# Kernel tuning notes

Hardware: AMD Instinct MI355X
Metric: run time of the kernel (lower is better)

The kernel has to match this reference:

```python
import jax, jax.numpy as jnp
import numpy as np


def setup_inputs() -> dict:
    key = jax.random.key(0)
    ks = jax.random.split(key, 6)
    B, S, D, E = 8, 4096, 4096, 64
    lim = 1.0 / np.sqrt(D)  # nn.Linear default init range
    return {
        "h": jax.random.normal(ks[0], (B, S, D), dtype=jnp.float32),
        "Ww": jax.random.uniform(ks[1], (E, D), dtype=jnp.float32, minval=-lim, maxval=lim),
        "bw": jax.random.uniform(ks[2], (E,), dtype=jnp.float32, minval=-lim, maxval=lim),
        "Wn": jax.random.uniform(ks[3], (E, D), dtype=jnp.float32, minval=-lim, maxval=lim),
        "bn": jax.random.uniform(ks[4], (E,), dtype=jnp.float32, minval=-lim, maxval=lim),
        "noise": jax.random.normal(ks[5], (B, S, E), dtype=jnp.float32),
        "top_k": 8,
    }


def reference(h, Ww, bw, Wn, bn, noise, top_k):
    B, S, E = h.shape[0], h.shape[1], Ww.shape[0]
    logits = jnp.einsum("bsd,ed->bse", h, Ww) + bw           # lin_w(h)
    noise_scale = jax.nn.softplus(jnp.einsum("bsd,ed->bse", h, Wn) + bn)  # softplus(lin_n(h))
    noisy = logits + noise * noise_scale
    full = jax.nn.softmax(noisy, axis=-1)
    topk, ix = jax.lax.top_k(noisy, top_k)                    # [B,S,k]
    # scatter topk values into a -inf tensor along the expert axis
    flat_noisy = noisy.reshape(-1, E)
    rows = jnp.arange(flat_noisy.shape[0])[:, None]           # [BS,1]
    sparse = jnp.full_like(flat_noisy, -jnp.inf).at[rows, ix.reshape(-1, top_k)].set(
        topk.reshape(-1, top_k))
    gates = jax.nn.softmax(sparse, axis=-1).reshape(B, S, E)
    return gates, ix, full
```

## Files before the change

kernel.cpp:

```cpp
#include <hip/hip_runtime.h>
#include <hip/hip_bf16.h>
#include <math.h>


typedef __attribute__((ext_vector_type(8))) _Float16 f16x8;
typedef __attribute__((ext_vector_type(4))) float f32x4;
typedef unsigned int u32;

#define BM 64
#define D_DIM 4096
#define NSTEP 128
#define WSTEP_BYTES 16384

#define BUF_BYTES 24576
#define SMEM_BYTES 49152

__device__ __forceinline__ float softplus_f(float x) {
    return fmaxf(x, 0.0f) + log1pf(expf(-fabsf(x)));
}

__device__ __forceinline__ void gl16(void* lds, const void* g) {
    __builtin_amdgcn_global_load_lds(
        (const __attribute__((address_space(1))) u32*)g,
        (__attribute__((address_space(3))) u32*)lds, 16, 0, 0);
}

#define MFMA16F(A, B, C) __builtin_amdgcn_mfma_f32_16x16x32_f16((A), (B), (C), 0, 0, 0)

__global__ __launch_bounds__(256)
void wconv_kernel(const float* __restrict__ Ww, const float* __restrict__ Wn,
                  char* __restrict__ Wp)
{
    const int bid = blockIdx.x;
    const int kc = bid >> 1, half = bid & 1;
    const int t = threadIdx.x;
    const int vrow = half * 64 + (t >> 2);
    const int c4 = t & 3;
    const float* src = (vrow < 64) ? (Ww + (size_t)vrow * D_DIM)
                                   : (Wn + (size_t)(vrow - 64) * D_DIM);
    const float4 a = *reinterpret_cast<const float4*>(src + kc * 32 + c4 * 8);
    const float4 b = *reinterpret_cast<const float4*>(src + kc * 32 + c4 * 8 + 4);
    const float f[8] = {a.x, a.y, a.z, a.w, b.x, b.y, b.z, b.w};
    union { _Float16 h[8]; uint4 q; } P0, P1;
#pragma unroll
    for (int i = 0; i < 8; ++i) {
        _Float16 lo = (_Float16)f[i];
        P0.h[i] = lo;
        P1.h[i] = (_Float16)((f[i] - (float)lo) * 2048.0f);
    }
    const int sc = c4 ^ ((vrow >> 2) & 3);
    char* dst = Wp + (size_t)kc * WSTEP_BYTES + vrow * 64 + sc * 16;
    *reinterpret_cast<uint4*>(dst)        = P0.q;
    *reinterpret_cast<uint4*>(dst + 8192) = P1.q;
}

__global__ __launch_bounds__(512, 4)
void router_kernel(const float* __restrict__ h,
                   const float* __restrict__ bw,
                   const float* __restrict__ bn,
                   const float* __restrict__ noise,
                   const char* __restrict__ Wp,
                   float* __restrict__ out_gates,
                   float* __restrict__ out_ix,
                   float* __restrict__ out_full)
{
    __shared__ __align__(16) char smem[SMEM_BYTES];

    const int t    = threadIdx.x;
    const int row0 = blockIdx.x * BM;
    const int lane = t & 63, w = t >> 6;
    const int c = lane & 15, kg = lane >> 4;
    const int wr = w >> 2, wc = w & 3;

    const int hl  = lane >> 3;
    const int hsc = (lane & 7) ^ hl;
    const float* hsrc = h + (size_t)(row0 + w * 8 + hl) * D_DIM + hsc * 4;
    const int hdst = w * 1024;
    const char* wsrc = Wp + w * 1024 + lane * 16;

    f32x4 grp[2][2], sA[2][2], accM[2][2], accM2[2][2];
#pragma unroll
    for (int fi = 0; fi < 2; ++fi)
#pragma unroll
        for (int j = 0; j < 2; ++j) {
            grp[fi][j] = (f32x4)0.0f; sA[fi][j] = (f32x4)0.0f;
            accM[fi][j] = (f32x4)0.0f; accM2[fi][j] = (f32x4)0.0f;
        }

    gl16(smem + hdst, hsrc);
    gl16(smem + 8192 + w * 1024, wsrc);
    gl16(smem + 8192 + 8192 + w * 1024, wsrc + 8192);
    __syncthreads();

    int cur = 0;
    for (int kc = 0; kc < NSTEP; ++kc) {
        if (kc + 1 < NSTEP) {
            char* nb = smem + (cur ^ 1) * BUF_BYTES;
            gl16(nb + hdst, hsrc + (size_t)(kc + 1) * 32);
            const char* ws = wsrc + (size_t)(kc + 1) * WSTEP_BYTES;
            gl16(nb + 8192 + w * 1024, ws);
            gl16(nb + 16384 + w * 1024, ws + 8192);
        }

        const char* hb = smem + cur * BUF_BYTES;
        const char* wb = hb + 8192;

        f16x8 A0[2], A1[2];
#pragma unroll
        for (int fi = 0; fi < 2; ++fi) {
            const int arow = wr * 32 + fi * 16 + c;
            const int s0 = ((kg * 2)     ^ (arow & 7)) * 16;
            const int s1 = ((kg * 2 + 1) ^ (arow & 7)) * 16;
            const float4 fa = *reinterpret_cast<const float4*>(hb + arow * 128 + s0);
            const float4 fb = *reinterpret_cast<const float4*>(hb + arow * 128 + s1);
            const float f[8] = {fa.x, fa.y, fa.z, fa.w, fb.x, fb.y, fb.z, fb.w};
#pragma unroll
            for (int i = 0; i < 8; ++i) {
                _Float16 lo = (_Float16)f[i];
                A0[fi][i] = lo;
                A1[fi][i] = (_Float16)((f[i] - (float)lo) * 2048.0f);
            }
        }

#pragma unroll
        for (int j = 0; j < 2; ++j) {
            const int brow = wc * 32 + j * 16 + c;
            const int bo = brow * 64 + ((kg ^ ((brow >> 2) & 3)) * 16);
            const f16x8 B0 = *reinterpret_cast<const f16x8*>(wb + bo);
            const f16x8 B1 = *reinterpret_cast<const f16x8*>(wb + bo + 8192);
#pragma unroll
            for (int fi = 0; fi < 2; ++fi) {
                grp[fi][j]   = MFMA16F(A0[fi], B0, grp[fi][j]);
                accM[fi][j]  = MFMA16F(A0[fi], B1, accM[fi][j]);
                accM[fi][j]  = MFMA16F(A1[fi], B0, accM[fi][j]);
                accM2[fi][j] = MFMA16F(A1[fi], B1, accM2[fi][j]);
            }
        }

        if ((kc & 15) == 15) {
#pragma unroll
            for (int fi = 0; fi < 2; ++fi)
#pragma unroll
                for (int j = 0; j < 2; ++j) {
#pragma unroll
                    for (int e = 0; e < 4; ++e) sA[fi][j][e] += grp[fi][j][e];
                    grp[fi][j] = (f32x4)0.0f;
                }
        }

        __syncthreads();
        cur ^= 1;
    }

    float* lw_s = reinterpret_cast<float*>(smem);
    float* ln_s = lw_s + 64 * 65;
    float* dst = (wc < 2) ? lw_s : ln_s;
#pragma unroll
    for (int fi = 0; fi < 2; ++fi)
#pragma unroll
        for (int j = 0; j < 2; ++j)
#pragma unroll
            for (int r = 0; r < 4; ++r) {
                const int rowl = wr * 32 + fi * 16 + kg * 4 + r;
                const int e = (wc & 1) * 32 + j * 16 + c;
                dst[rowl * 65 + e] = sA[fi][j][r]
                                   + accM[fi][j][r]  * 4.8828125e-4f
                                   + accM2[fi][j][r] * 2.384185791015625e-7f;
            }
    __syncthreads();

    const float bwv = bw[lane];
    const float bnv = bn[lane];
    for (int q = 0; q < 8; ++q) {
        const int lrow = w * 8 + q;
        const int grow = row0 + lrow;
        const float lwv = lw_s[lrow * 65 + lane] + bwv;
        const float lnv = ln_s[lrow * 65 + lane] + bnv;
        const float nz  = noise[(size_t)grow * 64 + lane];
        const float v   = lwv + nz * softplus_f(lnv);

        float cur2 = v;
        float m8 = 0.0f;
        int winIdx = 0;
        bool picked = false;
#pragma unroll
        for (int r = 0; r < 8; ++r) {
            float bvv = cur2;
            int   bi  = lane;
#pragma unroll
            for (int off = 32; off; off >>= 1) {
                const float ov = __shfl_xor(bvv, off);
                const int   oi = __shfl_xor(bi, off);
                if (ov > bvv || (ov == bvv && oi < bi)) { bvv = ov; bi = oi; }
            }
            if (r == 0) m8 = bvv;
            if (lane == r) winIdx = bi;
            if (lane == bi) { picked = true; cur2 = -INFINITY; }
        }

        const float pf = expf(v - m8);
        const float pg = picked ? pf : 0.0f;
        float sf = pf, sg = pg;
#pragma unroll
        for (int off = 32; off; off >>= 1) {
            sf += __shfl_xor(sf, off);
            sg += __shfl_xor(sg, off);
        }

        out_full [(size_t)grow * 64 + lane] = pf / sf;
        out_gates[(size_t)grow * 64 + lane] = pg / sg;
        if (lane < 8) out_ix[(size_t)grow * 8 + lane] = (float)winIdx;
    }
}

extern "C" void kernel_launch(void* const* d_in, const int* in_sizes, int n_in,
                              void* d_out, int out_size, void* d_ws, size_t ws_size,
                              hipStream_t stream) {
    const float* h  = (const float*)d_in[0];
    const float* Ww = (const float*)d_in[1];
    const float* bw = (const float*)d_in[2];
    const float* Wn = (const float*)d_in[3];
    const float* bn = (const float*)d_in[4];
    const float* nz = (const float*)d_in[5];

    const int rows = in_sizes[5] / 64;

    float* out = (float*)d_out;
    float* og = out;
    float* oi = out + (size_t)rows * 64;
    float* of = out + (size_t)rows * 64 + (size_t)rows * 8;

    char* Wp = (char*)d_ws;

    hipLaunchKernelGGL(wconv_kernel, dim3(256), dim3(256), 0, stream, Ww, Wn, Wp);
    hipLaunchKernelGGL(router_kernel, dim3(rows / BM), dim3(512), 0, stream,
                       h, bw, bn, nz, Wp, og, oi, of);
}
```

Before: 249.7 us.

## Triple-buffer LDS loads with partial waitcnt and drop lo*lo MFMA term

Measured after the change: 242.7 us, median of 2. 1.03x faster.

```diff
diff --git a/kernel.cpp b/kernel.cpp
--- a/kernel.cpp
+++ b/kernel.cpp
@@ -13,7 +13,7 @@
 #define WSTEP_BYTES 16384
 
 #define BUF_BYTES 24576
-#define SMEM_BYTES 49152
+#define SMEM_BYTES 73728
 
 __device__ __forceinline__ float softplus_f(float x) {
     return fmaxf(x, 0.0f) + log1pf(expf(-fabsf(x)));
@@ -78,31 +78,38 @@
     const int hdst = w * 1024;
     const char* wsrc = Wp + w * 1024 + lane * 16;
 
-    f32x4 grp[2][2], sA[2][2], accM[2][2], accM2[2][2];
+    f32x4 grp[2][2], sA[2][2], accM[2][2];
 #pragma unroll
     for (int fi = 0; fi < 2; ++fi)
 #pragma unroll
         for (int j = 0; j < 2; ++j) {
             grp[fi][j] = (f32x4)0.0f; sA[fi][j] = (f32x4)0.0f;
-            accM[fi][j] = (f32x4)0.0f; accM2[fi][j] = (f32x4)0.0f;
-        }
-
-    gl16(smem + hdst, hsrc);
-    gl16(smem + 8192 + w * 1024, wsrc);
-    gl16(smem + 8192 + 8192 + w * 1024, wsrc + 8192);
-    __syncthreads();
-
-    int cur = 0;
+            accM[fi][j] = (f32x4)0.0f;
+        }
+
+#pragma unroll
+    for (int p = 0; p < 2; ++p) {
+        char* nb = smem + p * BUF_BYTES;
+        gl16(nb + hdst, hsrc + (size_t)p * 32);
+        const char* ws = wsrc + (size_t)p * WSTEP_BYTES;
+        gl16(nb + 8192 + w * 1024, ws);
+        gl16(nb + 16384 + w * 1024, ws + 8192);
+    }
+    asm volatile("s_waitcnt vmcnt(3)" ::: "memory");
+    __builtin_amdgcn_sched_barrier(0);
+    __builtin_amdgcn_s_barrier();
+    __builtin_amdgcn_sched_barrier(0);
+
     for (int kc = 0; kc < NSTEP; ++kc) {
-        if (kc + 1 < NSTEP) {
-            char* nb = smem + (cur ^ 1) * BUF_BYTES;
-            gl16(nb + hdst, hsrc + (size_t)(kc + 1) * 32);
-            const char* ws = wsrc + (size_t)(kc + 1) * WSTEP_BYTES;
+        if (kc + 2 < NSTEP) {
+            char* nb = smem + ((kc + 2) % 3) * BUF_BYTES;
+            gl16(nb + hdst, hsrc + (size_t)(kc + 2) * 32);
+            const char* ws = wsrc + (size_t)(kc + 2) * WSTEP_BYTES;
             gl16(nb + 8192 + w * 1024, ws);
             gl16(nb + 16384 + w * 1024, ws + 8192);
         }
 
-        const char* hb = smem + cur * BUF_BYTES;
+        const char* hb = smem + (kc % 3) * BUF_BYTES;
         const char* wb = hb + 8192;
 
         f16x8 A0[2], A1[2];
@@ -130,10 +137,9 @@
             const f16x8 B1 = *reinterpret_cast<const f16x8*>(wb + bo + 8192);
 #pragma unroll
             for (int fi = 0; fi < 2; ++fi) {
-                grp[fi][j]   = MFMA16F(A0[fi], B0, grp[fi][j]);
-                accM[fi][j]  = MFMA16F(A0[fi], B1, accM[fi][j]);
-                accM[fi][j]  = MFMA16F(A1[fi], B0, accM[fi][j]);
-                accM2[fi][j] = MFMA16F(A1[fi], B1, accM2[fi][j]);
+                grp[fi][j]  = MFMA16F(A0[fi], B0, grp[fi][j]);
+                accM[fi][j] = MFMA16F(A0[fi], B1, accM[fi][j]);
+                accM[fi][j] = MFMA16F(A1[fi], B0, accM[fi][j]);
             }
         }
 
@@ -148,8 +154,14 @@
                 }
         }
 
-        __syncthreads();
-        cur ^= 1;
+        if (kc + 2 < NSTEP) {
+            asm volatile("s_waitcnt vmcnt(3)" ::: "memory");
+        } else {
+            asm volatile("s_waitcnt vmcnt(0)" ::: "memory");
+        }
+        __builtin_amdgcn_sched_barrier(0);
+        __builtin_amdgcn_s_barrier();
+        __builtin_amdgcn_sched_barrier(0);
     }
 
     float* lw_s = reinterpret_cast<float*>(smem);
@@ -163,9 +175,7 @@
             for (int r = 0; r < 4; ++r) {
                 const int rowl = wr * 32 + fi * 16 + kg * 4 + r;
                 const int e = (wc & 1) * 32 + j * 16 + c;
-                dst[rowl * 65 + e] = sA[fi][j][r]
-                                   + accM[fi][j][r]  * 4.8828125e-4f
-                                   + accM2[fi][j][r] * 2.384185791015625e-7f;
+                dst[rowl * 65 + e] = sA[fi][j][r] + accM[fi][j][r] * 4.8828125e-4f;
             }
     __syncthreads();
 
```

## Drop lo*lo split-fp16 MFMA term, shrink registers, raise occupancy to 6 waves

Applied to the files above, without the earlier changes.

New measurement: 318.5 us. +27.6%, slower.

```diff
diff --git a/kernel.cpp b/kernel.cpp
--- a/kernel.cpp
+++ b/kernel.cpp
@@ -54,7 +54,7 @@
     *reinterpret_cast<uint4*>(dst + 8192) = P1.q;
 }
 
-__global__ __launch_bounds__(512, 4)
+__global__ __launch_bounds__(512, 6)
 void router_kernel(const float* __restrict__ h,
                    const float* __restrict__ bw,
                    const float* __restrict__ bn,
@@ -78,62 +78,61 @@
     const int hdst = w * 1024;
     const char* wsrc = Wp + w * 1024 + lane * 16;
 
-    f32x4 grp[2][2], sA[2][2], accM[2][2], accM2[2][2];
+    f32x4 grp[2][2], sA[2][2], accM[2][2];
 #pragma unroll
     for (int fi = 0; fi < 2; ++fi)
 #pragma unroll
         for (int j = 0; j < 2; ++j) {
             grp[fi][j] = (f32x4)0.0f; sA[fi][j] = (f32x4)0.0f;
-            accM[fi][j] = (f32x4)0.0f; accM2[fi][j] = (f32x4)0.0f;
+            accM[fi][j] = (f32x4)0.0f;
         }
 
     gl16(smem + hdst, hsrc);
     gl16(smem + 8192 + w * 1024, wsrc);
-    gl16(smem + 8192 + 8192 + w * 1024, wsrc + 8192);
-    __syncthreads();
-
-    int cur = 0;
+    gl16(smem + 16384 + w * 1024, wsrc + 8192);
+    asm volatile("s_waitcnt vmcnt(0)" ::: "memory");
+    __builtin_amdgcn_sched_barrier(0);
+    __builtin_amdgcn_s_barrier();
+    __builtin_amdgcn_sched_barrier(0);
+
     for (int kc = 0; kc < NSTEP; ++kc) {
         if (kc + 1 < NSTEP) {
-            char* nb = smem + (cur ^ 1) * BUF_BYTES;
+            char* nb = smem + ((kc + 1) & 1) * BUF_BYTES;
             gl16(nb + hdst, hsrc + (size_t)(kc + 1) * 32);
             const char* ws = wsrc + (size_t)(kc + 1) * WSTEP_BYTES;
             gl16(nb + 8192 + w * 1024, ws);
             gl16(nb + 16384 + w * 1024, ws + 8192);
         }
 
-        const char* hb = smem + cur * BUF_BYTES;
+        const char* hb = smem + (kc & 1) * BUF_BYTES;
         const char* wb = hb + 8192;
 
-        f16x8 A0[2], A1[2];
 #pragma unroll
         for (int fi = 0; fi < 2; ++fi) {
-            const int arow = wr * 32 + fi * 16 + c;
-            const int s0 = ((kg * 2)     ^ (arow & 7)) * 16;
-            const int s1 = ((kg * 2 + 1) ^ (arow & 7)) * 16;
-            const float4 fa = *reinterpret_cast<const float4*>(hb + arow * 128 + s0);
-            const float4 fb = *reinterpret_cast<const float4*>(hb + arow * 128 + s1);
-            const float f[8] = {fa.x, fa.y, fa.z, fa.w, fb.x, fb.y, fb.z, fb.w};
-#pragma unroll
-            for (int i = 0; i < 8; ++i) {
-                _Float16 lo = (_Float16)f[i];
-                A0[fi][i] = lo;
-                A1[fi][i] = (_Float16)((f[i] - (float)lo) * 2048.0f);
-            }
-        }
-
-#pragma unroll
-        for (int j = 0; j < 2; ++j) {
-            const int brow = wc * 32 + j * 16 + c;
-            const int bo = brow * 64 + ((kg ^ ((brow >> 2) & 3)) * 16);
-            const f16x8 B0 = *reinterpret_cast<const f16x8*>(wb + bo);
-            const f16x8 B1 = *reinterpret_cast<const f16x8*>(wb + bo + 8192);
-#pragma unroll
-            for (int fi = 0; fi < 2; ++fi) {
-                grp[fi][j]   = MFMA16F(A0[fi], B0, grp[fi][j]);
-                accM[fi][j]  = MFMA16F(A0[fi], B1, accM[fi][j]);
-                accM[fi][j]  = MFMA16F(A1[fi], B0, accM[fi][j]);
-                accM2[fi][j] = MFMA16F(A1[fi], B1, accM2[fi][j]);
+            f16x8 A0f, A1f;
+            {
+                const int arow = wr * 32 + fi * 16 + c;
+                const int s0 = ((kg * 2)     ^ (arow & 7)) * 16;
+                const int s1 = ((kg * 2 + 1) ^ (arow & 7)) * 16;
+                const float4 fa = *reinterpret_cast<const float4*>(hb + arow * 128 + s0);
+                const float4 fb = *reinterpret_cast<const float4*>(hb + arow * 128 + s1);
+                const float f[8] = {fa.x, fa.y, fa.z, fa.w, fb.x, fb.y, fb.z, fb.w};
+#pragma unroll
+                for (int i = 0; i < 8; ++i) {
+                    _Float16 lo = (_Float16)f[i];
+                    A0f[i] = lo;
+                    A1f[i] = (_Float16)((f[i] - (float)lo) * 2048.0f);
+                }
+            }
+#pragma unroll
+            for (int j = 0; j < 2; ++j) {
+                const int brow = wc * 32 + j * 16 + c;
+                const int bo = brow * 64 + ((kg ^ ((brow >> 2) & 3)) * 16);
+                const f16x8 B0 = *reinterpret_cast<const f16x8*>(wb + bo);
+                const f16x8 B1 = *reinterpret_cast<const f16x8*>(wb + bo + 8192);
+                grp[fi][j]  = MFMA16F(A0f, B0, grp[fi][j]);
+                accM[fi][j] = MFMA16F(A0f, B1, accM[fi][j]);
+                accM[fi][j] = MFMA16F(A1f, B0, accM[fi][j]);
             }
         }
 
@@ -148,8 +147,10 @@
                 }
         }
 
-        __syncthreads();
-        cur ^= 1;
+        asm volatile("s_waitcnt vmcnt(0)" ::: "memory");
+        __builtin_amdgcn_sched_barrier(0);
+        __builtin_amdgcn_s_barrier();
+        __builtin_amdgcn_sched_barrier(0);
     }
 
     float* lw_s = reinterpret_cast<float*>(smem);
@@ -163,9 +164,7 @@
             for (int r = 0; r < 4; ++r) {
                 const int rowl = wr * 32 + fi * 16 + kg * 4 + r;
                 const int e = (wc & 1) * 32 + j * 16 + c;
-                dst[rowl * 65 + e] = sA[fi][j][r]
-                                   + accM[fi][j][r]  * 4.8828125e-4f
-                                   + accM2[fi][j][r] * 2.384185791015625e-7f;
+                dst[rowl * 65 + e] = sA[fi][j][r] + accM[fi][j][r] * 4.8828125e-4f;
             }
     __syncthreads();
 
```
